# Kernel optimization log

Measured on AMD Instinct MI355X. Metric: run time of the kernel, lower is better.

The kernel has to match this reference:

```python
import jax, jax.numpy as jnp
import numpy as np

N = 50000      # nodes
E = 800000     # edges (before self-loops)
DIN = 384
D = 128        # hidden_dim == output_dim
H = 4          # heads
FH = D // H    # per-head dim
B = 64         # graphs in batch
NEG = 0.2      # LeakyReLU slope in GATConv
EPS = 1e-5     # LayerNorm eps


def setup_inputs() -> dict:
    key = jax.random.key(0)
    ks = jax.random.split(key, 24)
    s = 0.02
    inp = {
        'node_features': jax.random.normal(ks[0], (N, DIN), jnp.float32),
        'edge_index': jax.random.randint(ks[1], (2, E), 0, N, dtype=jnp.int64),
        'edge_weight': jax.random.uniform(ks[2], (E,), jnp.float32),
        'batch': jnp.sort(jax.random.randint(ks[3], (N,), 0, B, dtype=jnp.int64)),
        # input projection
        'Wp': jax.random.normal(ks[4], (DIN, D), jnp.float32) * s,
        'bp': jnp.zeros((D,), jnp.float32),
    }
    for l in range(2):
        o = 5 + l * 9
        inp[f'W{l}'] = jax.random.normal(ks[o], (D, D), jnp.float32) * s      # lin_src (shared src/dst)
        inp[f'as{l}'] = jax.random.normal(ks[o + 1], (H, FH), jnp.float32) * s  # att_src
        inp[f'ad{l}'] = jax.random.normal(ks[o + 2], (H, FH), jnp.float32) * s  # att_dst
        inp[f'We{l}'] = jax.random.normal(ks[o + 3], (D,), jnp.float32) * s   # lin_edge (edge_dim=1)
        inp[f'ae{l}'] = jax.random.normal(ks[o + 4], (H, FH), jnp.float32) * s  # att_edge
        inp[f'b{l}'] = jnp.zeros((D,), jnp.float32)                           # GATConv bias
        inp[f'g{l}'] = jnp.ones((D,), jnp.float32)                            # LayerNorm gamma
        inp[f'be{l}'] = jnp.zeros((D,), jnp.float32)                          # LayerNorm beta
    return inp


def _gat(x, src, dst, ew, W, a_s, a_d, We, a_e, b):
    """PyG GATConv(in, D/H, heads=H, edge_dim=1), eval mode. ew includes self-loops."""
    n = x.shape[0]
    h = (x @ W).reshape(n, H, FH)                      # [N,H,FH]
    a_src = jnp.einsum('nhf,hf->nh', h, a_s)           # [N,H]
    a_dst = jnp.einsum('nhf,hf->nh', h, a_d)
    e = (ew[:, None] * We[None, :]).reshape(-1, H, FH)  # edge_dim=1 linear, no bias
    a_eg = jnp.einsum('ehf,hf->eh', e, a_e)            # [E,H]
    alpha = jax.nn.leaky_relu(a_src[src] + a_dst[dst] + a_eg, NEG)
    # softmax over incoming edges of each dst node
    amax = jax.ops.segment_max(alpha, dst, num_segments=n)
    amax = jnp.where(jnp.isfinite(amax), amax, 0.0)
    ex = jnp.exp(alpha - amax[dst])
    denom = jax.ops.segment_sum(ex, dst, num_segments=n)
    coef = ex / (denom[dst] + 1e-16)                   # [E,H]
    msg = h[src] * coef[..., None]                     # [E,H,FH]
    out = jax.ops.segment_sum(msg, dst, num_segments=n).reshape(n, D)
    return out + b


def _ln(x, g, b):
    mu = x.mean(-1, keepdims=True)
    v = ((x - mu) ** 2).mean(-1, keepdims=True)
    return (x - mu) * jax.lax.rsqrt(v + EPS) * g + b


def reference(node_features, edge_index, edge_weight, batch, Wp, bp,
              W0, as0, ad0, We0, ae0, b0, g0, be0,
              W1, as1, ad1, We1, ae1, b1, g1, be1):
    n = node_features.shape[0]
    # PyG GATConv add_self_loops=True, fill_value='mean' for edge_attr
    loop = jnp.arange(n, dtype=edge_index.dtype)
    src = jnp.concatenate([edge_index[0], loop])
    dst = jnp.concatenate([edge_index[1], loop])
    ew = jnp.concatenate([edge_weight, jnp.full((n,), edge_weight.mean(), edge_weight.dtype)])

    x = node_features @ Wp + bp
    for (W, a_s, a_d, We, a_e, b, g, be) in (
        (W0, as0, ad0, We0, ae0, b0, g0, be0),
        (W1, as1, ad1, We1, ae1, b1, g1, be1),
    ):
        res = x
        y = _gat(x, src, dst, ew, W, a_s, a_d, We, a_e, b)
        y = jax.nn.elu(_ln(y, g, be))
        x = y + res  # shapes match (hidden == output)

    # global_mean_pool
    s = jax.ops.segment_sum(x, batch, num_segments=B)
    c = jax.ops.segment_sum(jnp.ones((n,), x.dtype), batch, num_segments=B)
    return s / jnp.maximum(c, 1.0)[:, None]
```

## Files before the change

### kernel.cpp

```cpp
#include <hip/hip_runtime.h>

#define N_NODES 50000
#define N_EDGES 800000
#define DIN 384
#define DH 128
#define NB 64
#define NEG 0.2f

__device__ __forceinline__ float bf2f(unsigned short u) {
    return __uint_as_float((unsigned)u << 16);
}
__device__ __forceinline__ unsigned short f2bf(float x) {
    unsigned u = __float_as_uint(x);
    return (unsigned short)((u + 0x7fff + ((u >> 16) & 1)) >> 16);
}
__device__ __forceinline__ float sel4(float4 v, int k) {
    float r = v.x;
    r = (k == 1) ? v.y : r;
    r = (k == 2) ? v.z : r;
    r = (k == 3) ? v.w : r;
    return r;
}
using us8 = __attribute__((ext_vector_type(8))) unsigned short;
using short8 = __attribute__((ext_vector_type(8))) short;
using f32x4  = __attribute__((ext_vector_type(4))) float;

__global__ __launch_bounds__(256) void prep_w(const float* __restrict__ Wp,
        const float* __restrict__ W0, const float* __restrict__ W1,
        unsigned short* __restrict__ Wtp, unsigned short* __restrict__ Wt0,
        unsigned short* __restrict__ Wt1)
{
    const int i = blockIdx.x * 256 + threadIdx.x;
    if (i < DIN * DH) {
        const int k = i >> 7, n = i & 127;
        Wtp[(size_t)n * DIN + k] = f2bf(Wp[i]);
    }
    if (i < DH * DH) {
        const int k = i >> 7, n = i & 127;
        Wt0[(size_t)n * DH + k] = f2bf(W0[i]);
        Wt1[(size_t)n * DH + k] = f2bf(W1[i]);
    }
}

__global__ __launch_bounds__(256) void histew_kernel(const int* __restrict__ dst,
                                                     const float* __restrict__ ew,
                                                     int* __restrict__ cnt,
                                                     int* __restrict__ rank,
                                                     float* __restrict__ ews) {
    __shared__ float sred[4];
    const int tid = threadIdx.x;
    float v = 0.0f;
    for (int i = blockIdx.x * 256 + tid; i < N_EDGES; i += gridDim.x * 256) {
        rank[i] = atomicAdd(&cnt[dst[i]], 1);
        v += ew[i];
    }
    #pragma unroll
    for (int o = 32; o; o >>= 1) v += __shfl_down(v, o, 64);
    if ((tid & 63) == 0) sred[tid >> 6] = v;
    __syncthreads();
    if (tid == 0) atomicAdd(ews, sred[0] + sred[1] + sred[2] + sred[3]);
}

__global__ void scan_a(const int* __restrict__ cnt, int* __restrict__ scanned,
                       int* __restrict__ bsums) {
    __shared__ int s[256];
    int tid = threadIdx.x;
    int i = blockIdx.x * 256 + tid;
    int v = (i < N_NODES) ? cnt[i] : 0;
    s[tid] = v; __syncthreads();
    for (int o = 1; o < 256; o <<= 1) {
        int t = (tid >= o) ? s[tid - o] : 0;
        __syncthreads();
        s[tid] += t;
        __syncthreads();
    }
    if (i < N_NODES) scanned[i] = s[tid] - v;
    if (tid == 255) bsums[blockIdx.x] = s[255];
}

__global__ void scan_b(int* __restrict__ bsums, int nb,
                       const float* __restrict__ We0, const float* __restrict__ ae0,
                       const float* __restrict__ We1, const float* __restrict__ ae1,
                       const float* __restrict__ ews, float* __restrict__ consts) {
    __shared__ int s[256];
    int tid = threadIdx.x;
    int v = (tid < nb) ? bsums[tid] : 0;
    s[tid] = v; __syncthreads();
    for (int o = 1; o < 256; o <<= 1) {
        int t = (tid >= o) ? s[tid - o] : 0;
        __syncthreads();
        s[tid] += t;
        __syncthreads();
    }
    if (tid < nb) bsums[tid] = s[tid] - v;

    if (tid < 64) {
        const int l = tid;
        float p00 = We0[l] * ae0[l];
        float p01 = We0[l + 64] * ae0[l + 64];
        float p10 = We1[l] * ae1[l];
        float p11 = We1[l + 64] * ae1[l + 64];
        #pragma unroll
        for (int o = 1; o < 32; o <<= 1) {
            p00 += __shfl_xor(p00, o, 64); p01 += __shfl_xor(p01, o, 64);
            p10 += __shfl_xor(p10, o, 64); p11 += __shfl_xor(p11, o, 64);
        }
        const float c0 = __shfl(p00, 0, 64), c1 = __shfl(p00, 32, 64);
        const float c2 = __shfl(p01, 0, 64), c3 = __shfl(p01, 32, 64);
        const float d0 = __shfl(p10, 0, 64), d1 = __shfl(p10, 32, 64);
        const float d2 = __shfl(p11, 0, 64), d3 = __shfl(p11, 32, 64);
        if (l == 0) {
            consts[0] = c0; consts[1] = c1; consts[2] = c2; consts[3] = c3;
            consts[4] = d0; consts[5] = d1; consts[6] = d2; consts[7] = d3;
            consts[8] = ews[0] * (1.0f / N_EDGES);
        }
    }
}

__global__ void scan_c(const int* __restrict__ scanned, const int* __restrict__ bsums,
                       const int* __restrict__ cnt, int* __restrict__ ptr) {
    int i = blockIdx.x * 256 + threadIdx.x;
    if (i < N_NODES) {
        int p = scanned[i] + bsums[blockIdx.x];
        ptr[i] = p;
        if (i == N_NODES - 1) ptr[N_NODES] = p + cnt[i];
    }
}

__global__ __launch_bounds__(256) void fill_kernel(const int* __restrict__ src,
                            const int* __restrict__ dst,
                            const float* __restrict__ ew,
                            const int* __restrict__ rank,
                            const int* __restrict__ ptr,
                            int2* __restrict__ recE) {
    const int e0 = (blockIdx.x * 256 + threadIdx.x) * 4;
    if (e0 >= N_EDGES) return;
    const int4 d4 = *(const int4*)(dst + e0);
    const int4 s4 = *(const int4*)(src + e0);
    const int4 r4 = *(const int4*)(rank + e0);
    const float4 w4 = *(const float4*)(ew + e0);
    recE[ptr[d4.x] + r4.x] = make_int2(s4.x, __float_as_int(w4.x));
    recE[ptr[d4.y] + r4.y] = make_int2(s4.y, __float_as_int(w4.y));
    recE[ptr[d4.z] + r4.z] = make_int2(s4.z, __float_as_int(w4.z));
    recE[ptr[d4.w] + r4.w] = make_int2(s4.w, __float_as_int(w4.w));
}

__global__ __launch_bounds__(256) void mfma_gemm_proj(
    const float* __restrict__ A, const unsigned short* __restrict__ Wt,
    const float* __restrict__ bias, float* __restrict__ C,
    unsigned short* __restrict__ Cb, int M)
{
    constexpr int K = DIN, BM = 128, BK = 32, LS = 40;
    __shared__ unsigned short As[BM * LS];
    __shared__ unsigned short Bs[DH * LS];

    const int tid = threadIdx.x;
    const int w = tid >> 6, l = tid & 63;
    const int lane16 = l & 15, quad = l >> 4;
    const int m0 = blockIdx.x * BM;

    f32x4 acc[2][8] = {};

    const int ar = tid >> 1, ah = tid & 1;
    int arow = m0 + ar; if (arow >= M) arow = M - 1;
    const float* Ap = A + (size_t)arow * K;

    for (int k0 = 0; k0 < K; k0 += BK) {
        __syncthreads();
        #pragma unroll
        for (int j = 0; j < 4; ++j) {
            float4 v = *(const float4*)(Ap + k0 + ah * 16 + j * 4);
            ushort4 u = {f2bf(v.x), f2bf(v.y), f2bf(v.z), f2bf(v.w)};
            *(ushort4*)&As[ar * LS + ah * 16 + j * 4] = u;
        }
        #pragma unroll
        for (int i = 0; i < 2; ++i) {
            const int idx = tid + 256 * i;
            const int bn = idx >> 2, seg = idx & 3;
            us8 v = *(const us8*)(Wt + (size_t)bn * K + k0 + seg * 8);
            *(us8*)&Bs[bn * LS + seg * 8] = v;
        }
        __syncthreads();
        short8 af0 = *(short8*)&As[(w * 32 + lane16) * LS + quad * 8];
        short8 af1 = *(short8*)&As[(w * 32 + 16 + lane16) * LS + quad * 8];
        #pragma unroll
        for (int nt = 0; nt < 8; ++nt) {
            short8 bf = *(short8*)&Bs[(nt * 16 + lane16) * LS + quad * 8];
            acc[0][nt] = __builtin_amdgcn_mfma_f32_16x16x32_bf16(af0, bf, acc[0][nt], 0, 0, 0);
            acc[1][nt] = __builtin_amdgcn_mfma_f32_16x16x32_bf16(af1, bf, acc[1][nt], 0, 0, 0);
        }
    }

    #pragma unroll
    for (int r2 = 0; r2 < 2; ++r2) {
        const int orow0 = m0 + w * 32 + r2 * 16 + quad * 4;
        #pragma unroll
        for (int nt = 0; nt < 8; ++nt) {
            const int col = nt * 16 + lane16;
            const float bv = bias[col];
            #pragma unroll
            for (int r = 0; r < 4; ++r) {
                const int row = orow0 + r;
                if (row < M) {
                    const float v = acc[r2][nt][r] + bv;
                    C[(size_t)row * DH + col] = v;
                    Cb[(size_t)row * DH + col] = f2bf(v);
                }
            }
        }
    }
}

__global__ __launch_bounds__(256) void mfma_gemm_layer(
    const unsigned short* __restrict__ Ab, const unsigned short* __restrict__ Wt,
    unsigned short* __restrict__ Hout, int M,
    const float* __restrict__ a_s, const float* __restrict__ a_d,
    float* __restrict__ asrc_o, float* __restrict__ adst_o)
{
    constexpr int K = DH, BM = 64, BK = 32, LS = 40;
    __shared__ unsigned short As[BM * LS];
    __shared__ unsigned short Bs[DH * LS];

    const int tid = threadIdx.x;
    const int w = tid >> 6, l = tid & 63;
    const int lane16 = l & 15, quad = l >> 4;
    const int m0 = blockIdx.x * BM;

    f32x4 acc[8] = {};

    const int ar = tid >> 2, aseg = tid & 3;
    int arow = m0 + ar; if (arow >= M) arow = M - 1;
    const unsigned short* Ap = Ab + (size_t)arow * K;

    for (int k0 = 0; k0 < K; k0 += BK) {
        __syncthreads();
        {
            us8 v = *(const us8*)(Ap + k0 + aseg * 8);
            *(us8*)&As[ar * LS + aseg * 8] = v;
        }
        #pragma unroll
        for (int i = 0; i < 2; ++i) {
            const int idx = tid + 256 * i;
            const int bn = idx >> 2, seg = idx & 3;
            us8 v = *(const us8*)(Wt + (size_t)bn * K + k0 + seg * 8);
            *(us8*)&Bs[bn * LS + seg * 8] = v;
        }
        __syncthreads();
        short8 af = *(short8*)&As[(w * 16 + lane16) * LS + quad * 8];
        #pragma unroll
        for (int nt = 0; nt < 8; ++nt) {
            short8 bf = *(short8*)&Bs[(nt * 16 + lane16) * LS + quad * 8];
            acc[nt] = __builtin_amdgcn_mfma_f32_16x16x32_bf16(af, bf, acc[nt], 0, 0, 0);
        }
    }

    const int orow0 = m0 + w * 16 + quad * 4;
    #pragma unroll
    for (int nt = 0; nt < 8; ++nt) {
        const int col = nt * 16 + lane16;
        #pragma unroll
        for (int r = 0; r < 4; ++r) {
            const int row = orow0 + r;
            if (row < M)
                Hout[(size_t)row * DH + col] = f2bf(acc[nt][r]);
        }
    }

    float psh[4][4] = {}, pdh[4][4] = {};
    #pragma unroll
    for (int nt = 0; nt < 8; ++nt) {
        const int hd = nt >> 1;
        const float asv = a_s[nt * 16 + lane16];
        const float adv = a_d[nt * 16 + lane16];
        #pragma unroll
        for (int r = 0; r < 4; ++r) {
            psh[hd][r] = fmaf(acc[nt][r], asv, psh[hd][r]);
            pdh[hd][r] = fmaf(acc[nt][r], adv, pdh[hd][r]);
        }
    }
    #pragma unroll
    for (int o = 1; o < 16; o <<= 1) {
        #pragma unroll
        for (int hd = 0; hd < 4; ++hd)
            #pragma unroll
            for (int r = 0; r < 4; ++r) {
                psh[hd][r] += __shfl_xor(psh[hd][r], o, 64);
                pdh[hd][r] += __shfl_xor(pdh[hd][r], o, 64);
            }
    }
    if (lane16 == 0) {
        #pragma unroll
        for (int r = 0; r < 4; ++r) {
            const int row = orow0 + r;
            if (row < M) {
                float4 o1 = {psh[0][r], psh[1][r], psh[2][r], psh[3][r]};
                float4 o2 = {pdh[0][r], pdh[1][r], pdh[2][r], pdh[3][r]};
                *(float4*)(asrc_o + (size_t)row * 4) = o1;
                *(float4*)(adst_o + (size_t)row * 4) = o2;
            }
        }
    }
}

#define MSG_NPB 16
__global__ __launch_bounds__(256) void msg_kernel(
    const unsigned short* __restrict__ h, const float* __restrict__ asrc,
    const float* __restrict__ adst, const float* __restrict__ xres,
    const int* __restrict__ indptr, const int2* __restrict__ recE,
    const float* __restrict__ consts, const int layer,
    const float* __restrict__ bias, const float* __restrict__ gamma,
    const float* __restrict__ beta, float* __restrict__ xout,
    unsigned short* __restrict__ xob)
{
    const int l = threadIdx.x & 63;
    const int wv = threadIdx.x >> 6;
    const int grp = l >> 4;
    const int c8 = l & 15;
    const int hd8 = c8 >> 2;

    const int n = blockIdx.x * MSG_NPB + wv * 4 + grp;

    const float4 ccv = *(const float4*)(consts + layer * 4);
    const float cc_l = sel4(ccv, hd8);
    const float ewm = consts[8];
    const unsigned short* hb = h + c8 * 8;

    const int st = indptr[n];
    const int deg = indptr[n + 1] - st;
    const float ad_l = adst[(size_t)n * 4 + hd8];
    const float as_l = asrc[(size_t)n * 4 + hd8];

    float a0 = as_l + ad_l + ewm * cc_l;
    a0 = a0 > 0.f ? a0 : NEG * a0;
    const float pv0_l = __expf(a0);

    float dsum = 0.f;
    float acc8[8];
    {
        us8 u = *(const us8*)(hb + (size_t)n * DH);
        #pragma unroll
        for (int i = 0; i < 8; ++i) acc8[i] = pv0_l * bf2f(u[i]);
    }

    const int2* rq = recE + st;
    int e = 0;
    for (; e + 3 < deg; e += 4) {
        const int2 r0 = rq[e],     r1 = rq[e + 1];
        const int2 r2 = rq[e + 2], r3 = rq[e + 3];
        const float av0 = asrc[(size_t)r0.x * 4 + hd8];
        const float av1 = asrc[(size_t)r1.x * 4 + hd8];
        const float av2 = asrc[(size_t)r2.x * 4 + hd8];
        const float av3 = asrc[(size_t)r3.x * 4 + hd8];
        us8 u0 = *(const us8*)(hb + (size_t)r0.x * DH);
        us8 u1 = *(const us8*)(hb + (size_t)r1.x * DH);
        us8 u2 = *(const us8*)(hb + (size_t)r2.x * DH);
        us8 u3 = *(const us8*)(hb + (size_t)r3.x * DH);
        float al0 = av0 + ad_l + __int_as_float(r0.y) * cc_l;
        float al1 = av1 + ad_l + __int_as_float(r1.y) * cc_l;
        float al2 = av2 + ad_l + __int_as_float(r2.y) * cc_l;
        float al3 = av3 + ad_l + __int_as_float(r3.y) * cc_l;
        al0 = al0 > 0.f ? al0 : NEG * al0;
        al1 = al1 > 0.f ? al1 : NEG * al1;
        al2 = al2 > 0.f ? al2 : NEG * al2;
        al3 = al3 > 0.f ? al3 : NEG * al3;
        const float c0 = __expf(al0), c1 = __expf(al1);
        const float c2 = __expf(al2), c3 = __expf(al3);
        dsum += (c0 + c1) + (c2 + c3);
        #pragma unroll
        for (int i = 0; i < 8; ++i)
            acc8[i] = fmaf(c0, bf2f(u0[i]),
                      fmaf(c1, bf2f(u1[i]),
                      fmaf(c2, bf2f(u2[i]),
                      fmaf(c3, bf2f(u3[i]), acc8[i]))));
    }
    for (; e < deg; ++e) {
        const int2 r = rq[e];
        const float av = asrc[(size_t)r.x * 4 + hd8];
        us8 u = *(const us8*)(hb + (size_t)r.x * DH);
        float al = av + ad_l + __int_as_float(r.y) * cc_l;
        al = al > 0.f ? al : NEG * al;
        const float c = __expf(al);
        dsum += c;
        #pragma unroll
        for (int i = 0; i < 8; ++i) acc8[i] = fmaf(c, bf2f(u[i]), acc8[i]);
    }

    const float inv_d = 1.0f / (dsum + pv0_l + 1e-16f);
    const float4 b4a = *(const float4*)(bias + c8 * 8);
    const float4 b4b = *(const float4*)(bias + c8 * 8 + 4);
    float y[8];
    y[0] = acc8[0] * inv_d + b4a.x; y[1] = acc8[1] * inv_d + b4a.y;
    y[2] = acc8[2] * inv_d + b4a.z; y[3] = acc8[3] * inv_d + b4a.w;
    y[4] = acc8[4] * inv_d + b4b.x; y[5] = acc8[5] * inv_d + b4b.y;
    y[6] = acc8[6] * inv_d + b4b.z; y[7] = acc8[7] * inv_d + b4b.w;

    float s1 = 0.f, s2 = 0.f;
    #pragma unroll
    for (int i = 0; i < 8; ++i) { s1 += y[i]; s2 += y[i] * y[i]; }
    #pragma unroll
    for (int o = 1; o < 16; o <<= 1) {
        s1 += __shfl_xor(s1, o, 64);
        s2 += __shfl_xor(s2, o, 64);
    }
    const float mu = s1 * (1.0f / DH);
    const float var = s2 * (1.0f / DH) - mu * mu;
    const float rs = rsqrtf(var + 1e-5f);

    const float4 g4a = *(const float4*)(gamma + c8 * 8);
    const float4 g4b = *(const float4*)(gamma + c8 * 8 + 4);
    const float4 e4a = *(const float4*)(beta + c8 * 8);
    const float4 e4b = *(const float4*)(beta + c8 * 8 + 4);
    const float4 r4a = *(const float4*)(xres + (size_t)n * DH + c8 * 8);
    const float4 r4b = *(const float4*)(xres + (size_t)n * DH + c8 * 8 + 4);
    const float gv[8] = {g4a.x, g4a.y, g4a.z, g4a.w, g4b.x, g4b.y, g4b.z, g4b.w};
    const float ev[8] = {e4a.x, e4a.y, e4a.z, e4a.w, e4b.x, e4b.y, e4b.z, e4b.w};
    const float rv[8] = {r4a.x, r4a.y, r4a.z, r4a.w, r4b.x, r4b.y, r4b.z, r4b.w};
    float z[8];
    #pragma unroll
    for (int i = 0; i < 8; ++i) {
        float t = (y[i] - mu) * rs * gv[i] + ev[i];
        z[i] = (t > 0.f ? t : __expf(t) - 1.0f) + rv[i];
    }
    *(float4*)(xout + (size_t)n * DH + c8 * 8)     = *(float4*)&z[0];
    *(float4*)(xout + (size_t)n * DH + c8 * 8 + 4) = *(float4*)&z[4];
    if (xob) {
        ushort4 ub0 = {f2bf(z[0]), f2bf(z[1]), f2bf(z[2]), f2bf(z[3])};
        ushort4 ub1 = {f2bf(z[4]), f2bf(z[5]), f2bf(z[6]), f2bf(z[7])};
        *(ushort4*)(xob + (size_t)n * DH + c8 * 8)     = ub0;
        *(ushort4*)(xob + (size_t)n * DH + c8 * 8 + 4) = ub1;
    }
}

#define PNODES 64
__global__ __launch_bounds__(128) void pool_kernel(const float* __restrict__ x,
        const int* __restrict__ batch, float* __restrict__ pool, int* __restrict__ gcnt)
{
    int t = threadIdx.x;
    int n0 = blockIdx.x * PNODES;
    if (n0 >= N_NODES) return;
    int n1 = min(n0 + PNODES, N_NODES);
    float acc = 0.f; int cn = 0;
    int curb = batch[n0];
    for (int n = n0; n < n1; ++n) {
        int b = batch[n];
        if (b != curb) {
            atomicAdd(&pool[(size_t)curb * DH + t], acc);
            if (t == 0) atomicAdd(&gcnt[curb], cn);
            acc = 0.f; cn = 0; curb = b;
        }
        acc += x[(size_t)n * DH + t];
        ++cn;
    }
    atomicAdd(&pool[(size_t)curb * DH + t], acc);
    if (t == 0) atomicAdd(&gcnt[curb], cn);
}

__global__ void div_kernel(const float* __restrict__ pool, const int* __restrict__ gcnt,
                           float* __restrict__ out)
{
    int i = blockIdx.x * blockDim.x + threadIdx.x;
    if (i < NB * DH) {
        float c = (float)gcnt[i >> 7];
        out[i] = pool[i] / fmaxf(c, 1.0f);
    }
}

extern "C" void kernel_launch(void* const* d_in, const int* in_sizes, int n_in,
                              void* d_out, int out_size, void* d_ws, size_t ws_size,
                              hipStream_t stream)
{
    const float* nf    = (const float*)d_in[0];
    const int*   esrc  = (const int*)d_in[1];
    const int*   edst  = esrc + N_EDGES;
    const float* ew    = (const float*)d_in[2];
    const int*   batch = (const int*)d_in[3];
    const float* Wp    = (const float*)d_in[4];
    const float* bp    = (const float*)d_in[5];
    const float* Wl[2]  = {(const float*)d_in[6],  (const float*)d_in[14]};
    const float* asl[2] = {(const float*)d_in[7],  (const float*)d_in[15]};
    const float* adl[2] = {(const float*)d_in[8],  (const float*)d_in[16]};
    const float* Wel[2] = {(const float*)d_in[9],  (const float*)d_in[17]};
    const float* ael[2] = {(const float*)d_in[10], (const float*)d_in[18]};
    const float* bl[2]  = {(const float*)d_in[11], (const float*)d_in[19]};
    const float* gl[2]  = {(const float*)d_in[12], (const float*)d_in[20]};
    const float* bel[2] = {(const float*)d_in[13], (const float*)d_in[21]};
    float* outp = (float*)d_out;

    char* w = (char*)d_ws;
    auto alloc = [&](size_t bytes) { char* p = w; w += (bytes + 255) & ~255ull; return p; };
    float* xA     = (float*)alloc((size_t)N_NODES * DH * 4);
    float* xB     = (float*)alloc((size_t)N_NODES * DH * 4);
    unsigned short* hbuf = (unsigned short*)alloc((size_t)N_NODES * DH * 2);
    unsigned short* xb   = (unsigned short*)alloc((size_t)N_NODES * DH * 2);
    float* asrc   = (float*)alloc((size_t)N_NODES * 4 * 4);
    float* adst   = (float*)alloc((size_t)N_NODES * 4 * 4);
    float* pool   = (float*)alloc((size_t)NB * DH * 4);
    int* gcnt     = (int*)alloc(256);
    float* ews    = (float*)alloc(256);
    int* cnt      = (int*)alloc((size_t)N_NODES * 4);
    int* scanned  = (int*)alloc((size_t)N_NODES * 4);
    int* bsums    = (int*)alloc(1024);
    int* ptr      = (int*)alloc((size_t)(N_NODES + 8) * 4);
    int* rank     = (int*)alloc((size_t)N_EDGES * 4);
    int2* recE    = (int2*)alloc((size_t)N_EDGES * 8);
    float* consts = (float*)alloc(256);
    unsigned short* Wtp = (unsigned short*)alloc((size_t)DH * DIN * 2);
    unsigned short* Wt0 = (unsigned short*)alloc((size_t)DH * DH * 2);
    unsigned short* Wt1 = (unsigned short*)alloc((size_t)DH * DH * 2);
    unsigned short* Wts[2] = {Wt0, Wt1};

    hipMemsetAsync(pool, 0, (size_t)NB * DH * 4 + 256 + 256 + (size_t)N_NODES * 4, stream);

    const int sb = (N_NODES + 255) / 256;

    prep_w<<<(DIN * DH + 255) / 256, 256, 0, stream>>>(Wp, Wl[0], Wl[1], Wtp, Wt0, Wt1);
    histew_kernel<<<1024, 256, 0, stream>>>(edst, ew, cnt, rank, ews);
    scan_a<<<sb, 256, 0, stream>>>(cnt, scanned, bsums);
    scan_b<<<1, 256, 0, stream>>>(bsums, sb, Wel[0], ael[0], Wel[1], ael[1], ews, consts);
    scan_c<<<sb, 256, 0, stream>>>(scanned, bsums, cnt, ptr);
    fill_kernel<<<(N_EDGES / 4 + 255) / 256, 256, 0, stream>>>(esrc, edst, ew, rank, ptr, recE);

    mfma_gemm_proj<<<(N_NODES + 127) / 128, 256, 0, stream>>>(nf, Wtp, bp, xA, xb, N_NODES);

    const int gb = (N_NODES + 63) / 64;
    const float* xin = xA;
    float* xout = xB;
    for (int l = 0; l < 2; ++l) {
        mfma_gemm_layer<<<gb, 256, 0, stream>>>(xb, Wts[l], hbuf, N_NODES,
                                                asl[l], adl[l], asrc, adst);
        msg_kernel<<<N_NODES / MSG_NPB, 256, 0, stream>>>(
            hbuf, asrc, adst, xin, ptr, recE, consts, l,
            bl[l], gl[l], bel[l], xout, (l == 0) ? xb : nullptr);
        float* tmp = (float*)xin; xin = xout; xout = tmp;
    }

    pool_kernel<<<(N_NODES + PNODES - 1) / PNODES, 128, 0, stream>>>(xin, batch, pool, gcnt);
    div_kernel<<<(NB * DH + 255) / 256, 256, 0, stream>>>(pool, gcnt, outp);
}
```

Before: 374.1 us.

## Merge preprocessing kernels and fuse mean-pool into last message kernel

Folds the weight bf16 transposition into the histogram kernel, merges the scan stages into two kernels (each block sums its own prefix of block sums), and runs the CSR fill and the input projection GEMM as disjoint block ranges of one launch. The last layer's message kernel now accumulates per-graph sums in shared memory and atomically adds them into the pool, so the final node features are never written out or read back. The aim is fewer launches and less memory traffic, in exchange for extra shared memory and per-block atomics in the message kernel, which may lower its occupancy.

```diff
diff --git a/kernel.cpp b/kernel.cpp
--- a/kernel.cpp
+++ b/kernel.cpp
@@ -25,30 +25,28 @@
 using short8 = __attribute__((ext_vector_type(8))) short;
 using f32x4  = __attribute__((ext_vector_type(4))) float;
 
-__global__ __launch_bounds__(256) void prep_w(const float* __restrict__ Wp,
-        const float* __restrict__ W0, const float* __restrict__ W1,
-        unsigned short* __restrict__ Wtp, unsigned short* __restrict__ Wt0,
-        unsigned short* __restrict__ Wt1)
-{
-    const int i = blockIdx.x * 256 + threadIdx.x;
-    if (i < DIN * DH) {
-        const int k = i >> 7, n = i & 127;
-        Wtp[(size_t)n * DIN + k] = f2bf(Wp[i]);
-    }
-    if (i < DH * DH) {
-        const int k = i >> 7, n = i & 127;
-        Wt0[(size_t)n * DH + k] = f2bf(W0[i]);
-        Wt1[(size_t)n * DH + k] = f2bf(W1[i]);
-    }
-}
-
 __global__ __launch_bounds__(256) void histew_kernel(const int* __restrict__ dst,
                                                      const float* __restrict__ ew,
                                                      int* __restrict__ cnt,
                                                      int* __restrict__ rank,
-                                                     float* __restrict__ ews) {
+                                                     float* __restrict__ ews,
+                                                     const float* __restrict__ Wp,
+                                                     const float* __restrict__ W0,
+                                                     const float* __restrict__ W1,
+                                                     unsigned short* __restrict__ Wtp,
+                                                     unsigned short* __restrict__ Wt0,
+                                                     unsigned short* __restrict__ Wt1) {
     __shared__ float sred[4];
     const int tid = threadIdx.x;
+    const int pi = blockIdx.x * 256 + tid;
+    if (blockIdx.x < 192) {
+        const int k = pi >> 7, n = pi & 127;
+        Wtp[(size_t)n * DIN + k] = f2bf(Wp[pi]);
+        if (pi < DH * DH) {
+            Wt0[(size_t)n * DH + k] = f2bf(W0[pi]);
+            Wt1[(size_t)n * DH + k] = f2bf(W1[pi]);
+        }
+    }
     float v = 0.0f;
     for (int i = blockIdx.x * 256 + tid; i < N_EDGES; i += gridDim.x * 256) {
         rank[i] = atomicAdd(&cnt[dst[i]], 1);
@@ -61,40 +59,27 @@
     if (tid == 0) atomicAdd(ews, sred[0] + sred[1] + sred[2] + sred[3]);
 }
 
-__global__ void scan_a(const int* __restrict__ cnt, int* __restrict__ scanned,
-                       int* __restrict__ bsums) {
-    __shared__ int s[256];
-    int tid = threadIdx.x;
-    int i = blockIdx.x * 256 + tid;
-    int v = (i < N_NODES) ? cnt[i] : 0;
-    s[tid] = v; __syncthreads();
-    for (int o = 1; o < 256; o <<= 1) {
-        int t = (tid >= o) ? s[tid - o] : 0;
-        __syncthreads();
-        s[tid] += t;
-        __syncthreads();
-    }
-    if (i < N_NODES) scanned[i] = s[tid] - v;
-    if (tid == 255) bsums[blockIdx.x] = s[255];
-}
-
-__global__ void scan_b(int* __restrict__ bsums, int nb,
+#define SB 196
+__global__ __launch_bounds__(256) void scan_a(const int* __restrict__ cnt,
+                       int* __restrict__ scanned, int* __restrict__ bsums,
                        const float* __restrict__ We0, const float* __restrict__ ae0,
                        const float* __restrict__ We1, const float* __restrict__ ae1,
                        const float* __restrict__ ews, float* __restrict__ consts) {
     __shared__ int s[256];
-    int tid = threadIdx.x;
-    int v = (tid < nb) ? bsums[tid] : 0;
-    s[tid] = v; __syncthreads();
-    for (int o = 1; o < 256; o <<= 1) {
-        int t = (tid >= o) ? s[tid - o] : 0;
-        __syncthreads();
-        s[tid] += t;
-        __syncthreads();
-    }
-    if (tid < nb) bsums[tid] = s[tid] - v;
-
-    if (tid < 64) {
+    const int tid = threadIdx.x;
+    if (blockIdx.x < SB) {
+        int i = blockIdx.x * 256 + tid;
+        int v = (i < N_NODES) ? cnt[i] : 0;
+        s[tid] = v; __syncthreads();
+        for (int o = 1; o < 256; o <<= 1) {
+            int t = (tid >= o) ? s[tid - o] : 0;
+            __syncthreads();
+            s[tid] += t;
+            __syncthreads();
+        }
+        if (i < N_NODES) scanned[i] = s[tid] - v;
+        if (tid == 255) bsums[blockIdx.x] = s[255];
+    } else if (tid < 64) {
         const int l = tid;
         float p00 = We0[l] * ae0[l];
         float p01 = We0[l + 64] * ae0[l + 64];
@@ -117,35 +102,31 @@
     }
 }
 
-__global__ void scan_c(const int* __restrict__ scanned, const int* __restrict__ bsums,
-                       const int* __restrict__ cnt, int* __restrict__ ptr) {
-    int i = blockIdx.x * 256 + threadIdx.x;
+__global__ __launch_bounds__(256) void scan_bc(const int* __restrict__ scanned,
+                        const int* __restrict__ bsums,
+                        const int* __restrict__ cnt, int* __restrict__ ptr) {
+    __shared__ int red[4];
+    const int tid = threadIdx.x;
+    int part = 0;
+    for (int j = tid; j < blockIdx.x; j += 256) part += bsums[j];
+    #pragma unroll
+    for (int o = 32; o; o >>= 1) part += __shfl_down(part, o, 64);
+    if ((tid & 63) == 0) red[tid >> 6] = part;
+    __syncthreads();
+    const int off = red[0] + red[1] + red[2] + red[3];
+    const int i = blockIdx.x * 256 + tid;
     if (i < N_NODES) {
-        int p = scanned[i] + bsums[blockIdx.x];
+        const int p = scanned[i] + off;
         ptr[i] = p;
         if (i == N_NODES - 1) ptr[N_NODES] = p + cnt[i];
     }
 }
 
-__global__ __launch_bounds__(256) void fill_kernel(const int* __restrict__ src,
-                            const int* __restrict__ dst,
-                            const float* __restrict__ ew,
-                            const int* __restrict__ rank,
-                            const int* __restrict__ ptr,
-                            int2* __restrict__ recE) {
-    const int e0 = (blockIdx.x * 256 + threadIdx.x) * 4;
-    if (e0 >= N_EDGES) return;
-    const int4 d4 = *(const int4*)(dst + e0);
-    const int4 s4 = *(const int4*)(src + e0);
-    const int4 r4 = *(const int4*)(rank + e0);
-    const float4 w4 = *(const float4*)(ew + e0);
-    recE[ptr[d4.x] + r4.x] = make_int2(s4.x, __float_as_int(w4.x));
-    recE[ptr[d4.y] + r4.y] = make_int2(s4.y, __float_as_int(w4.y));
-    recE[ptr[d4.z] + r4.z] = make_int2(s4.z, __float_as_int(w4.z));
-    recE[ptr[d4.w] + r4.w] = make_int2(s4.w, __float_as_int(w4.w));
-}
-
-__global__ __launch_bounds__(256) void mfma_gemm_proj(
+#define PROJB 391
+__global__ __launch_bounds__(256) void fillproj_kernel(
+    const int* __restrict__ src, const int* __restrict__ dst,
+    const float* __restrict__ ew, const int* __restrict__ rank,
+    const int* __restrict__ ptr, int2* __restrict__ recE,
     const float* __restrict__ A, const unsigned short* __restrict__ Wt,
     const float* __restrict__ bias, float* __restrict__ C,
     unsigned short* __restrict__ Cb, int M)
@@ -153,8 +134,22 @@
     constexpr int K = DIN, BM = 128, BK = 32, LS = 40;
     __shared__ unsigned short As[BM * LS];
     __shared__ unsigned short Bs[DH * LS];
-
     const int tid = threadIdx.x;
+
+    if (blockIdx.x >= PROJB) {
+        const int e0 = ((blockIdx.x - PROJB) * 256 + tid) * 4;
+        if (e0 >= N_EDGES) return;
+        const int4 d4 = *(const int4*)(dst + e0);
+        const int4 s4 = *(const int4*)(src + e0);
+        const int4 r4 = *(const int4*)(rank + e0);
+        const float4 w4 = *(const float4*)(ew + e0);
+        recE[ptr[d4.x] + r4.x] = make_int2(s4.x, __float_as_int(w4.x));
+        recE[ptr[d4.y] + r4.y] = make_int2(s4.y, __float_as_int(w4.y));
+        recE[ptr[d4.z] + r4.z] = make_int2(s4.z, __float_as_int(w4.z));
+        recE[ptr[d4.w] + r4.w] = make_int2(s4.w, __float_as_int(w4.w));
+        return;
+    }
+
     const int w = tid >> 6, l = tid & 63;
     const int lane16 = l & 15, quad = l >> 4;
     const int m0 = blockIdx.x * BM;
@@ -303,6 +298,7 @@
 }
 
 #define MSG_NPB 16
+template<bool POOL>
 __global__ __launch_bounds__(256) void msg_kernel(
     const unsigned short* __restrict__ h, const float* __restrict__ asrc,
     const float* __restrict__ adst, const float* __restrict__ xres,
@@ -310,15 +306,26 @@
     const float* __restrict__ consts, const int layer,
     const float* __restrict__ bias, const float* __restrict__ gamma,
     const float* __restrict__ beta, float* __restrict__ xout,
-    unsigned short* __restrict__ xob)
+    unsigned short* __restrict__ xob,
+    const int* __restrict__ batch, float* __restrict__ pool,
+    int* __restrict__ gcnt)
 {
+    __shared__ float pacc[16][DH];
+    __shared__ int sb[16], firstb[16], scnt[16], nsl;
+
     const int l = threadIdx.x & 63;
     const int wv = threadIdx.x >> 6;
     const int grp = l >> 4;
     const int c8 = l & 15;
     const int hd8 = c8 >> 2;
 
-    const int n = blockIdx.x * MSG_NPB + wv * 4 + grp;
+    const int ninb = wv * 4 + grp;
+    const int n = blockIdx.x * MSG_NPB + ninb;
+
+    if constexpr (POOL) {
+        if (c8 == 0) sb[ninb] = batch[n];
+        for (int t = threadIdx.x; t < 16 * DH; t += 256) ((float*)pacc)[t] = 0.f;
+    }
 
     const float4 ccv = *(const float4*)(consts + layer * 4);
     const float cc_l = sel4(ccv, hd8);
@@ -421,38 +428,39 @@
         float t = (y[i] - mu) * rs * gv[i] + ev[i];
         z[i] = (t > 0.f ? t : __expf(t) - 1.0f) + rv[i];
     }
-    *(float4*)(xout + (size_t)n * DH + c8 * 8)     = *(float4*)&z[0];
-    *(float4*)(xout + (size_t)n * DH + c8 * 8 + 4) = *(float4*)&z[4];
-    if (xob) {
+
+    if constexpr (!POOL) {
+        *(float4*)(xout + (size_t)n * DH + c8 * 8)     = *(float4*)&z[0];
+        *(float4*)(xout + (size_t)n * DH + c8 * 8 + 4) = *(float4*)&z[4];
         ushort4 ub0 = {f2bf(z[0]), f2bf(z[1]), f2bf(z[2]), f2bf(z[3])};
         ushort4 ub1 = {f2bf(z[4]), f2bf(z[5]), f2bf(z[6]), f2bf(z[7])};
         *(ushort4*)(xob + (size_t)n * DH + c8 * 8)     = ub0;
         *(ushort4*)(xob + (size_t)n * DH + c8 * 8 + 4) = ub1;
-    }
-}
-
-#define PNODES 64
-__global__ __launch_bounds__(128) void pool_kernel(const float* __restrict__ x,
-        const int* __restrict__ batch, float* __restrict__ pool, int* __restrict__ gcnt)
-{
-    int t = threadIdx.x;
-    int n0 = blockIdx.x * PNODES;
-    if (n0 >= N_NODES) return;
-    int n1 = min(n0 + PNODES, N_NODES);
-    float acc = 0.f; int cn = 0;
-    int curb = batch[n0];
-    for (int n = n0; n < n1; ++n) {
-        int b = batch[n];
-        if (b != curb) {
-            atomicAdd(&pool[(size_t)curb * DH + t], acc);
-            if (t == 0) atomicAdd(&gcnt[curb], cn);
-            acc = 0.f; cn = 0; curb = b;
-        }
-        acc += x[(size_t)n * DH + t];
-        ++cn;
-    }
-    atomicAdd(&pool[(size_t)curb * DH + t], acc);
-    if (t == 0) atomicAdd(&gcnt[curb], cn);
+    } else {
+        __syncthreads();
+        int slot = 0;
+        #pragma unroll 1
+        for (int j = 1; j <= ninb; ++j) slot += (sb[j] != sb[j - 1]);
+        #pragma unroll
+        for (int k = 0; k < 8; ++k) atomicAdd(&pacc[slot][c8 * 8 + k], z[k]);
+        if (threadIdx.x == 0) {
+            int s = 0, c = 1;
+            firstb[0] = sb[0];
+            for (int j = 1; j < 16; ++j) {
+                if (sb[j] != sb[j - 1]) { scnt[s] = c; ++s; firstb[s] = sb[j]; c = 1; }
+                else ++c;
+            }
+            scnt[s] = c; nsl = s + 1;
+        }
+        __syncthreads();
+        const int ns = nsl;
+        for (int s = 0; s < ns; ++s) {
+            if (threadIdx.x < DH)
+                atomicAdd(&pool[(size_t)firstb[s] * DH + threadIdx.x], pacc[s][threadIdx.x]);
+            if (threadIdx.x == 0)
+                atomicAdd(&gcnt[firstb[s]], scnt[s]);
+        }
+    }
 }
 
 __global__ void div_kernel(const float* __restrict__ pool, const int* __restrict__ gcnt,
@@ -511,29 +519,28 @@
 
     hipMemsetAsync(pool, 0, (size_t)NB * DH * 4 + 256 + 256 + (size_t)N_NODES * 4, stream);
 
-    const int sb = (N_NODES + 255) / 256;
-
-    prep_w<<<(DIN * DH + 255) / 256, 256, 0, stream>>>(Wp, Wl[0], Wl[1], Wtp, Wt0, Wt1);
-    histew_kernel<<<1024, 256, 0, stream>>>(edst, ew, cnt, rank, ews);
-    scan_a<<<sb, 256, 0, stream>>>(cnt, scanned, bsums);
-    scan_b<<<1, 256, 0, stream>>>(bsums, sb, Wel[0], ael[0], Wel[1], ael[1], ews, consts);
-    scan_c<<<sb, 256, 0, stream>>>(scanned, bsums, cnt, ptr);
-    fill_kernel<<<(N_EDGES / 4 + 255) / 256, 256, 0, stream>>>(esrc, edst, ew, rank, ptr, recE);
-
-    mfma_gemm_proj<<<(N_NODES + 127) / 128, 256, 0, stream>>>(nf, Wtp, bp, xA, xb, N_NODES);
+    histew_kernel<<<1024, 256, 0, stream>>>(edst, ew, cnt, rank, ews,
+                                            Wp, Wl[0], Wl[1], Wtp, Wt0, Wt1);
+    scan_a<<<SB + 1, 256, 0, stream>>>(cnt, scanned, bsums,
+                                       Wel[0], ael[0], Wel[1], ael[1], ews, consts);
+    scan_bc<<<SB, 256, 0, stream>>>(scanned, bsums, cnt, ptr);
+    fillproj_kernel<<<PROJB + (N_EDGES / 4 + 255) / 256, 256, 0, stream>>>(
+        esrc, edst, ew, rank, ptr, recE, nf, Wtp, bp, xA, xb, N_NODES);
 
     const int gb = (N_NODES + 63) / 64;
-    const float* xin = xA;
-    float* xout = xB;
-    for (int l = 0; l < 2; ++l) {
-        mfma_gemm_layer<<<gb, 256, 0, stream>>>(xb, Wts[l], hbuf, N_NODES,
-                                                asl[l], adl[l], asrc, adst);
-        msg_kernel<<<N_NODES / MSG_NPB, 256, 0, stream>>>(
-            hbuf, asrc, adst, xin, ptr, recE, consts, l,
-            bl[l], gl[l], bel[l], xout, (l == 0) ? xb : nullptr);
-        float* tmp = (float*)xin; xin = xout; xout = tmp;
-    }
-
-    pool_kernel<<<(N_NODES + PNODES - 1) / PNODES, 128, 0, stream>>>(xin, batch, pool, gcnt);
+    const int mb = N_NODES / MSG_NPB;
+
+    mfma_gemm_layer<<<gb, 256, 0, stream>>>(xb, Wts[0], hbuf, N_NODES,
+                                            asl[0], adl[0], asrc, adst);
+    msg_kernel<false><<<mb, 256, 0, stream>>>(
+        hbuf, asrc, adst, xA, ptr, recE, consts, 0,
+        bl[0], gl[0], bel[0], xB, xb, nullptr, nullptr, nullptr);
+
+    mfma_gemm_layer<<<gb, 256, 0, stream>>>(xb, Wts[1], hbuf, N_NODES,
+                                            asl[1], adl[1], asrc, adst);
+    msg_kernel<true><<<mb, 256, 0, stream>>>(
+        hbuf, asrc, adst, xB, ptr, recE, consts, 1,
+        bl[1], gl[1], bel[1], nullptr, nullptr, batch, pool, gcnt);
+
     div_kernel<<<(NB * DH + 255) / 256, 256, 0, stream>>>(pool, gcnt, outp);
 }
```

New measurement: 379.6 us. No clear change (+1.5%).
